# Optimization experiments

Measured on AMD Instinct MI355X. Metric: run time of the kernel, lower is better.

## Reference

```python
import jax, jax.numpy as jnp
import numpy as np

NUM_GRAPHS = 128
NUM_LAYERS = 3
D_IN = 64
D_H = 64
D_OUT = 10
N_NODES = 100000
N_EDGES = 1000000


def segment_softmax(scores, seg, num_segments):
    # numerically stable softmax over variable-size segments (per-destination-node)
    m = jax.ops.segment_max(scores, seg, num_segments=num_segments)
    ex = jnp.exp(scores - m[seg])
    s = jax.ops.segment_sum(ex, seg, num_segments=num_segments)
    return ex / (s[seg] + 1e-16)


def setup_inputs() -> dict:
    key = jax.random.key(0)
    ks = jax.random.split(key, 16)
    x = jax.random.normal(ks[0], (N_NODES, D_IN), dtype=jnp.float32)
    edge_index = jax.random.randint(ks[1], (2, N_EDGES), 0, N_NODES, dtype=jnp.int32)
    batch = jnp.sort(jax.random.randint(ks[2], (N_NODES,), 0, NUM_GRAPHS, dtype=jnp.int32))
    s = 0.05
    # stacked per-layer TransformerConv params (input_dim == hidden_dim so shapes align)
    Wq = jax.random.normal(ks[3], (NUM_LAYERS, D_H, D_H), dtype=jnp.float32) * s
    bq = jnp.zeros((NUM_LAYERS, D_H), dtype=jnp.float32)
    Wk = jax.random.normal(ks[4], (NUM_LAYERS, D_H, D_H), dtype=jnp.float32) * s
    bk = jnp.zeros((NUM_LAYERS, D_H), dtype=jnp.float32)
    Wv = jax.random.normal(ks[5], (NUM_LAYERS, D_H, D_H), dtype=jnp.float32) * s
    bv = jnp.zeros((NUM_LAYERS, D_H), dtype=jnp.float32)
    Ws = jax.random.normal(ks[6], (NUM_LAYERS, D_H, D_H), dtype=jnp.float32) * s  # root/skip lin
    bs = jnp.zeros((NUM_LAYERS, D_H), dtype=jnp.float32)
    W1 = jax.random.normal(ks[7], (D_H, D_H), dtype=jnp.float32) * s
    b1 = jnp.zeros((D_H,), dtype=jnp.float32)
    W2 = jax.random.normal(ks[8], (D_H, D_OUT), dtype=jnp.float32) * s
    b2 = jnp.zeros((D_OUT,), dtype=jnp.float32)
    return {"x": x, "edge_index": edge_index, "batch": batch,
            "Wq": Wq, "bq": bq, "Wk": Wk, "bk": bk, "Wv": Wv, "bv": bv,
            "Ws": Ws, "bs": bs, "W1": W1, "b1": b1, "W2": W2, "b2": b2}


def reference(x, edge_index, batch, Wq, bq, Wk, bk, Wv, bv, Ws, bs, W1, b1, W2, b2):
    n = x.shape[0]
    src, dst = edge_index[0], edge_index[1]  # PyG: edge_index[0]=source j, [1]=target i
    scale = 1.0 / jnp.sqrt(jnp.asarray(D_H, x.dtype))
    h = x
    pooled = []
    for l in range(NUM_LAYERS):
        q = h @ Wq[l] + bq[l]          # [N, d] query of target node
        k = h @ Wk[l] + bk[l]          # [N, d] key of source node
        v = h @ Wv[l] + bv[l]          # [N, d] value of source node
        scores = jnp.sum(q[dst] * k[src], axis=-1) * scale          # [E]
        alpha = segment_softmax(scores, dst, n)                     # softmax over in-edges
        agg = jax.ops.segment_sum(v[src] * alpha[:, None], dst, num_segments=n)  # [N, d]
        h = jax.nn.relu(agg + h @ Ws[l] + bs[l])                    # root_weight skip + relu
        pooled.append(jax.ops.segment_sum(h, batch, num_segments=NUM_GRAPHS))   # global_add_pool
    pooled_st = jnp.stack(pooled)                                   # [L, G, d]
    p = jax.nn.relu(pooled_st[-1] @ W1 + b1)                        # dropout p=0 / eval
    out = p @ W2 + b2                                               # [G, D_OUT]
    return out, pooled_st
```

## Files before the change

kernel.cpp:

```cpp
#include <hip/hip_runtime.h>
#include <hip/hip_bf16.h>
#include <math.h>

#define NN 100000
#define NE 1000000
#define DD 64
#define NG 128
#define NL 3

#define NBUK 196
#define EPB 2048
#define NBLK ((NE + EPB - 1) / EPB)
#define BCAP 6144
#define NDC 64

typedef unsigned short ushort_t;
typedef unsigned int u32;
typedef __attribute__((ext_vector_type(8))) short short8v;
typedef __attribute__((ext_vector_type(2))) float f32x2;
typedef __attribute__((ext_vector_type(4))) float f32x4;
typedef __attribute__((ext_vector_type(4))) unsigned int u32x4;

__device__ __forceinline__ ushort_t f2bf(float f) {
    __hip_bfloat16 h = __float2bfloat16(f);
    return *reinterpret_cast<ushort_t*>(&h);
}
__device__ __forceinline__ unsigned cvtpk(float lo, float hi) {
    unsigned r;
    asm("v_cvt_pk_bf16_f32 %0, %1, %2" : "=v"(r) : "v"(lo), "v"(hi));
    return r;
}
__device__ __forceinline__ f32x2 bfpair(u32 u) {
    f32x2 r;
    r.x = __builtin_bit_cast(float, u << 16);
    r.y = __builtin_bit_cast(float, u & 0xffff0000u);
    return r;
}
template <bool HI>
__device__ __forceinline__ f32x2 f8pair(u32 u) {
    return __builtin_amdgcn_cvt_pk_f32_fp8(u, HI);
}
__device__ __forceinline__ float sum8(float x) {
    int v = __builtin_bit_cast(int, x);
    x += __builtin_bit_cast(float, __builtin_amdgcn_update_dpp(0, v, 0xB1, 0xF, 0xF, true));
    v = __builtin_bit_cast(int, x);
    x += __builtin_bit_cast(float, __builtin_amdgcn_update_dpp(0, v, 0x4E, 0xF, 0xF, true));
    v = __builtin_bit_cast(int, x);
    x += __builtin_bit_cast(float, __builtin_amdgcn_update_dpp(0, v, 0x141, 0xF, 0xF, true));
    return x;
}


__global__ __launch_bounds__(256) void zero_k(float* __restrict__ out, int totOut,
                                              int* __restrict__ gcur, int* __restrict__ gdh) {
    int i = blockIdx.x * 256 + threadIdx.x;
    if (i < totOut) out[i] = 0.f;
    if (blockIdx.x == 0 && threadIdx.x < NBUK) gcur[threadIdx.x] = 0;
    if (blockIdx.x == 1 && threadIdx.x < NDC) gdh[threadIdx.x] = 0;
}


__global__ __launch_bounds__(256) void fused_k(const float* __restrict__ x, ushort_t* __restrict__ hbf,
                                               const float* __restrict__ Wq, const float* __restrict__ Wk,
                                               const float* __restrict__ Wv, const float* __restrict__ Ws_,
                                               ushort_t* __restrict__ wpack,
                                               const int* __restrict__ src, const int* __restrict__ dst,
                                               u32* __restrict__ binbuf, int* __restrict__ gcur,
                                               int cvtBlocks) {
    __shared__ int hist[NBUK];
    __shared__ int excl[NBUK];
    __shared__ int cur[NBUK];
    __shared__ int gbase[NBUK];
    __shared__ int tmp[256];
    __shared__ u32 pairs[EPB];
    __shared__ unsigned char bukid[EPB];

    int b = blockIdx.x, t = threadIdx.x;
    if (b < cvtBlocks) {
        int base = (b * 256 + t) * 4;
        float4 v = *(const float4*)&x[base];
        uint2 pk;
        pk.x = cvtpk(v.x, v.y);
        pk.y = cvtpk(v.z, v.w);
        *(uint2*)&hbf[base] = pk;
        return;
    }
    b -= cvtBlocks;
    if (b < NL * 4) {
        if (t < 64) {
            int mat = b & 3, layer = b >> 2;
            const float* W = ((mat == 0) ? Wq : (mat == 1) ? Wk : (mat == 2) ? Wv : Ws_) + layer * DD * DD;
#pragma unroll
            for (int ct = 0; ct < 4; ct++)
#pragma unroll
                for (int ks = 0; ks < 2; ks++)
#pragma unroll
                    for (int j = 0; j < 8; j++) {
                        float v = W[(ks * 32 + (t >> 4) * 8 + j) * DD + ct * 16 + (t & 15)];
                        wpack[((size_t)(b * 8 + ct * 2 + ks)) * 512 + t * 8 + j] = f2bf(v);
                    }
        }
        return;
    }
    b -= NL * 4;
    int e0 = b * EPB;
    int totvalid = NE - e0; if (totvalid > EPB) totvalid = EPB;

    for (int i = t; i < NBUK; i += 256) hist[i] = 0;
    __syncthreads();

    int mysrc[8], mydst[8];
#pragma unroll
    for (int i = 0; i < 8; i++) {
        int e = e0 + i * 256 + t;
        bool v = e < NE;
        mysrc[i] = v ? src[e] : -1;
        mydst[i] = v ? dst[e] : -1;
        if (v) atomicAdd(&hist[mydst[i] >> 9], 1);
    }
    __syncthreads();

    int v = (t < NBUK) ? hist[t] : 0;
    tmp[t] = v;
    __syncthreads();
#pragma unroll
    for (int off = 1; off < 256; off <<= 1) {
        int a = (t >= off) ? tmp[t - off] : 0;
        __syncthreads();
        tmp[t] += a;
        __syncthreads();
    }
    if (t < NBUK) { excl[t] = tmp[t] - v; cur[t] = tmp[t] - v; }
    __syncthreads();

#pragma unroll
    for (int i = 0; i < 8; i++) {
        if (mydst[i] >= 0) {
            int bb = mydst[i] >> 9;
            int p = atomicAdd(&cur[bb], 1);
            pairs[p] = ((u32)(mydst[i] & 511) << 17) | (u32)mysrc[i];
            bukid[p] = (unsigned char)bb;
        }
    }
    if (t < NBUK && v > 0) gbase[t] = atomicAdd(&gcur[t], v);
    __syncthreads();

    for (int i = t; i < totvalid; i += 256) {
        int bb = bukid[i];
        int idx = gbase[bb] + (i - excl[bb]);
        if (idx < BCAP) binbuf[(size_t)bb * BCAP + idx] = pairs[i];
    }
}


__global__ __launch_bounds__(256) void csr_k(const u32* __restrict__ binbuf,
                                             const int* __restrict__ gcur,
                                             int* __restrict__ rowstart,
                                             int* __restrict__ csr_src,
                                             int* __restrict__ gdh) {
    __shared__ u32 pairs[BCAP];
    __shared__ int csrb[BCAP];
    __shared__ int deg[512];
    __shared__ int excl[512];
    __shared__ int cur[512];
    __shared__ int tmp[512];
    __shared__ int bt[256];
    __shared__ int ch[NDC];
    int b = blockIdx.x;
    int t = threadIdx.x;

    int bv = 0;
    if (t < NBUK) { bv = gcur[t]; if (bv > BCAP) bv = BCAP; }
    bt[t] = bv;
    __syncthreads();
#pragma unroll
    for (int off = 1; off < 256; off <<= 1) {
        int a = (t >= off) ? bt[t - off] : 0;
        __syncthreads();
        bt[t] += a;
        __syncthreads();
    }
    int base = (b == 0) ? 0 : bt[b - 1];
    int T = bt[b] - base;
    if (b == 0 && t == 0) rowstart[NN] = bt[NBUK - 1];
    int nbase = b << 9;

    for (int i = t; i < 512; i += 256) deg[i] = 0;
    if (t < NDC) ch[t] = 0;
    for (int i = t; i < T; i += 256) pairs[i] = binbuf[(size_t)b * BCAP + i];
    __syncthreads();
    for (int i = t; i < T; i += 256) atomicAdd(&deg[pairs[i] >> 17], 1);
    __syncthreads();

    for (int i = t; i < 512; i += 256) {
        if (nbase + i < NN) {
            int d = deg[i]; if (d > NDC - 1) d = NDC - 1;
            atomicAdd(&ch[d], 1);
        }
    }

    int v0 = deg[t], v1 = deg[t + 256];
    tmp[t] = v0; tmp[t + 256] = v1;
    __syncthreads();
#pragma unroll
    for (int off = 1; off < 512; off <<= 1) {
        int a0 = (t >= off) ? tmp[t - off] : 0;
        int i1 = t + 256;
        int a1 = (i1 >= off) ? tmp[i1 - off] : 0;
        __syncthreads();
        tmp[t] += a0; tmp[i1] += a1;
        __syncthreads();
    }
    excl[t] = tmp[t] - v0; excl[t + 256] = tmp[t + 256] - v1;
    cur[t] = excl[t]; cur[t + 256] = excl[t + 256];
    if (t < NDC && ch[t]) atomicAdd(&gdh[t], ch[t]);
    __syncthreads();

    for (int i = t; i < 512; i += 256) {
        int n = nbase + i;
        if (n < NN) rowstart[n] = base + excl[i];
    }

    for (int i = t; i < T; i += 256) {
        u32 p = pairs[i];
        int pos = atomicAdd(&cur[p >> 17], 1);
        csrb[pos] = (int)(p & 0x1FFFFu);
    }
    __syncthreads();
    for (int i = t; i < T; i += 256) csr_src[base + i] = csrb[i];
}


__global__ __launch_bounds__(64) void dscan_k(const int* __restrict__ gdh,
                                              int* __restrict__ gdcur) {
    int t = threadIdx.x;
    int v = gdh[t];
    int inc = v;
#pragma unroll
    for (int off = 1; off < NDC; off <<= 1) {
        int u = __shfl_up(inc, off);
        if (t >= off) inc += u;
    }
    gdcur[t] = inc - v;
}

__global__ __launch_bounds__(256) void dperm_k(const int* __restrict__ rowstart,
                                               int* __restrict__ gdcur,
                                               int* __restrict__ perm) {
    __shared__ int h[NDC];
    __shared__ int cur[NDC];
    int t = threadIdx.x;
    if (t < NDC) h[t] = 0;
    __syncthreads();
    int n0 = blockIdx.x * 1024;
    int myd[4];
#pragma unroll
    for (int i = 0; i < 4; i++) {
        int n = n0 + i * 256 + t;
        myd[i] = -1;
        if (n < NN) {
            int d = rowstart[n + 1] - rowstart[n];
            if (d > NDC - 1) d = NDC - 1;
            myd[i] = d;
            atomicAdd(&h[d], 1);
        }
    }
    __syncthreads();
    if (t < NDC) cur[t] = h[t] ? atomicAdd(&gdcur[t], h[t]) : 0;
    __syncthreads();
#pragma unroll
    for (int i = 0; i < 4; i++) {
        if (myd[i] >= 0) {
            int pos = atomicAdd(&cur[myd[i]], 1);
            perm[pos] = n0 + i * 256 + t;
        }
    }
}


__global__ __launch_bounds__(256) void gemm4_k(const ushort_t* __restrict__ hbf,
                                               const ushort_t* __restrict__ wpl,
                                               const float* __restrict__ bq_, const float* __restrict__ bk_,
                                               const float* __restrict__ bv_, const float* __restrict__ bs_,
                                               ushort_t* __restrict__ qo, unsigned char* __restrict__ kv8,
                                               ushort_t* __restrict__ so) {
    int t = threadIdx.x;
    int lane = t & 63, wv = t >> 6;
    int ln = lane & 15, lq = lane >> 4;
    int rowbase = blockIdx.x * 64;

    const float* bsel = (wv == 0) ? bq_ : (wv == 1) ? bk_ : (wv == 2) ? bv_ : bs_;
    ushort_t* osel    = (wv == 0) ? qo : so;
    int kvoff = (wv == 1) ? 0 : 64;

    short8v wfrag[4][2];
#pragma unroll
    for (int ct = 0; ct < 4; ct++)
#pragma unroll
        for (int ks = 0; ks < 2; ks++)
            wfrag[ct][ks] = *(const short8v*)&wpl[((size_t)(wv * 8 + ct * 2 + ks)) * 512 + lane * 8];

    float4 bias[4];
#pragma unroll
    for (int ct = 0; ct < 4; ct++) bias[ct] = *(const float4*)&bsel[ct * 16 + lq * 4];

#pragma unroll
    for (int rt = 0; rt < 4; rt++) {
        int grow = rowbase + rt * 16 + ln;
        bool rv = grow < NN;
        int gr = rv ? grow : NN - 1;
        short8v h0 = *(const short8v*)&hbf[(size_t)gr * DD + lq * 8];
        short8v h1 = *(const short8v*)&hbf[(size_t)gr * DD + 32 + lq * 8];
#pragma unroll
        for (int ct = 0; ct < 4; ct++) {
            f32x4 acc;
            acc[0] = bias[ct].x; acc[1] = bias[ct].y; acc[2] = bias[ct].z; acc[3] = bias[ct].w;
            acc = __builtin_amdgcn_mfma_f32_16x16x32_bf16(wfrag[ct][0], h0, acc, 0, 0, 0);
            acc = __builtin_amdgcn_mfma_f32_16x16x32_bf16(wfrag[ct][1], h1, acc, 0, 0, 0);
            if (rv) {
                if (wv == 1 || wv == 2) {
                    int pk8 = __builtin_amdgcn_cvt_pk_fp8_f32(acc[0], acc[1], 0, false);
                    pk8 = __builtin_amdgcn_cvt_pk_fp8_f32(acc[2], acc[3], pk8, true);
                    *(u32*)&kv8[(size_t)grow * 128 + kvoff + ct * 16 + lq * 4] = (u32)pk8;
                } else {
                    uint2 pk;
                    pk.x = cvtpk(acc[0], acc[1]);
                    pk.y = cvtpk(acc[2], acc[3]);
                    *(uint2*)&osel[(size_t)grow * DD + ct * 16 + lq * 4] = pk;
                }
            }
        }
    }
}


#define SCLOG2E 0.18033688011112042f

__global__ __launch_bounds__(256) void agg_k(const ushort_t* __restrict__ qb,
                                             const unsigned char* __restrict__ kv8,
                                             const ushort_t* __restrict__ skb,
                                             const int* __restrict__ rowstart,
                                             const int* __restrict__ csr_src,
                                             const int* __restrict__ perm,
                                             ushort_t* __restrict__ hout) {
    int wv = threadIdx.x >> 6, lane = threadIdx.x & 63;
    int g = lane >> 3, j = lane & 7, sub = g & 1;
    int slot = blockIdx.x * 16 + wv * 4 + (g >> 1);
    if (slot >= NN) return;
    int nid = perm[(NN - 1) - slot];
    int r0 = rowstart[nid];
    int r1 = rowstart[nid + 1];

    u32x4 qa = *(const u32x4*)(qb + ((u32)nid << 6) + ((u32)j << 3));
    f32x2 q0 = bfpair(qa.x), q1 = bfpair(qa.y), q2 = bfpair(qa.z), q3 = bfpair(qa.w);

    float m = -1.0e38f, se = 0.f;
    f32x2 a0 = {0.f, 0.f}, a1 = {0.f, 0.f}, a2 = {0.f, 0.f}, a3 = {0.f, 0.f};

    int clampE = r1 - 1; if (clampE < 0) clampE = 0;
    int e0 = r0 + sub, e1 = e0 + 2;
    int s0 = csr_src[e0 < clampE ? e0 : clampE];
    int s1 = csr_src[e1 < clampE ? e1 : clampE];
    uint2 k0 = *(const uint2*)(kv8 + (size_t)s0 * 128 + 8 * j);
    uint2 v0 = *(const uint2*)(kv8 + (size_t)s0 * 128 + 64 + 8 * j);
    uint2 k1 = *(const uint2*)(kv8 + (size_t)s1 * 128 + 8 * j);
    uint2 v1 = *(const uint2*)(kv8 + (size_t)s1 * 128 + 64 + 8 * j);

    while (__ballot(e0 < r1)) {
        int e2 = e1 + 2;
        int s2 = csr_src[e2 < clampE ? e2 : clampE];
        uint2 k2 = *(const uint2*)(kv8 + (size_t)s2 * 128 + 8 * j);
        uint2 v2 = *(const uint2*)(kv8 + (size_t)s2 * 128 + 64 + 8 * j);

        f32x2 dp2 = q0 * f8pair<false>(k0.x);
        dp2 += q1 * f8pair<true >(k0.x);
        dp2 += q2 * f8pair<false>(k0.y);
        dp2 += q3 * f8pair<true >(k0.y);
        float dp = sum8(dp2.x + dp2.y);

        float w = 0.f;
        if (e0 < r1) {
            float sc = dp * SCLOG2E;
            if (sc <= m + 11.5f) { w = exp2f(sc - m); }
            else {
                float cc = exp2f(m - sc);
                se *= cc; a0 *= cc; a1 *= cc; a2 *= cc; a3 *= cc;
                m = sc; w = 1.f;
            }
        }
        se += w;
        a0 += f8pair<false>(v0.x) * w;
        a1 += f8pair<true >(v0.x) * w;
        a2 += f8pair<false>(v0.y) * w;
        a3 += f8pair<true >(v0.y) * w;

        e0 = e1; e1 = e2;
        k0 = k1; v0 = v1; k1 = k2; v1 = v2;
    }

    float M = fmaxf(m, __shfl_xor(m, 8));
    float cc = exp2f(m - M);
    se *= cc; a0 *= cc; a1 *= cc; a2 *= cc; a3 *= cc;
    se += __shfl_xor(se, 8);
    a0.x += __shfl_xor(a0.x, 8); a0.y += __shfl_xor(a0.y, 8);
    a1.x += __shfl_xor(a1.x, 8); a1.y += __shfl_xor(a1.y, 8);
    a2.x += __shfl_xor(a2.x, 8); a2.y += __shfl_xor(a2.y, 8);
    a3.x += __shfl_xor(a3.x, 8); a3.y += __shfl_xor(a3.y, 8);

    if (sub == 0) {
        float inv = 1.0f / (se + 1e-16f);
        u32x4 sk = *(const u32x4*)(skb + ((u32)nid << 6) + ((u32)j << 3));
        f32x2 o0 = a0 * inv + bfpair(sk.x);
        f32x2 o1 = a1 * inv + bfpair(sk.y);
        f32x2 o2 = a2 * inv + bfpair(sk.z);
        f32x2 o3 = a3 * inv + bfpair(sk.w);
        u32x4 pk;
        pk.x = cvtpk(fmaxf(o0.x, 0.f), fmaxf(o0.y, 0.f));
        pk.y = cvtpk(fmaxf(o1.x, 0.f), fmaxf(o1.y, 0.f));
        pk.z = cvtpk(fmaxf(o2.x, 0.f), fmaxf(o2.y, 0.f));
        pk.w = cvtpk(fmaxf(o3.x, 0.f), fmaxf(o3.y, 0.f));
        *(u32x4*)(hout + ((u32)nid << 6) + ((u32)j << 3)) = pk;
    }
}


#define POOL_ROWS 128

__global__ __launch_bounds__(256) void pool_k(const ushort_t* __restrict__ h,
                                              const int* __restrict__ batch,
                                              float* __restrict__ pooled) {
    int i0 = blockIdx.x * POOL_ROWS;
    int i1 = i0 + POOL_ROWS; if (i1 > NN) i1 = NN;
    int lane = threadIdx.x & 63;
    int wv = threadIdx.x >> 6;
    float acc = 0.f;
    int gcur = -1;
    for (int i = i0 + wv; i < i1; i += 4) {
        int gi = batch[i];
        if (gi != gcur) {
            if (gcur >= 0) atomicAdd(&pooled[gcur * DD + lane], acc);
            gcur = gi; acc = 0.f;
        }
        unsigned u = ((unsigned)h[(size_t)i * DD + lane]) << 16;
        acc += __builtin_bit_cast(float, u);
    }
    if (gcur >= 0) atomicAdd(&pooled[gcur * DD + lane], acc);
}


__global__ __launch_bounds__(64) void head_k(const float* __restrict__ pooled2,
                                             const float* __restrict__ W1,
                                             const float* __restrict__ b1,
                                             const float* __restrict__ W2,
                                             const float* __restrict__ b2,
                                             float* __restrict__ out) {
    int g = blockIdx.x;
    int c = threadIdx.x;
    __shared__ float pg[64], p[64];
    pg[c] = pooled2[g * DD + c];
    __syncthreads();
    float a = b1[c];
#pragma unroll 8
    for (int kk = 0; kk < 64; kk++) a += pg[kk] * W1[kk * DD + c];
    p[c] = fmaxf(a, 0.f);
    __syncthreads();
    if (c < 10) {
        float o = b2[c];
#pragma unroll 8
        for (int kk = 0; kk < 64; kk++) o += p[kk] * W2[kk * 10 + c];
        out[g * 10 + c] = o;
    }
}


extern "C" void kernel_launch(void* const* d_in, const int* in_sizes, int n_in,
                              void* d_out, int out_size, void* d_ws, size_t ws_size,
                              hipStream_t stream) {
    const float* x    = (const float*)d_in[0];
    const int*   ei   = (const int*)d_in[1];
    const int*   batch= (const int*)d_in[2];
    const float* Wq   = (const float*)d_in[3];
    const float* bq   = (const float*)d_in[4];
    const float* Wk   = (const float*)d_in[5];
    const float* bk   = (const float*)d_in[6];
    const float* Wv   = (const float*)d_in[7];
    const float* bv   = (const float*)d_in[8];
    const float* Wsp  = (const float*)d_in[9];
    const float* bsp  = (const float*)d_in[10];
    const float* W1   = (const float*)d_in[11];
    const float* b1   = (const float*)d_in[12];
    const float* W2   = (const float*)d_in[13];
    const float* b2   = (const float*)d_in[14];
    float* out = (float*)d_out;
    float* pooled = out + NG * 10;

    const int* srcv = ei;
    const int* dstv = ei + NE;

    const size_t NEL = (size_t)NN * DD;
    ushort_t* hbf = (ushort_t*)d_ws;
    ushort_t* qb  = hbf + NEL;
    ushort_t* skb = qb  + NEL;
    unsigned char* kv8 = (unsigned char*)(skb + NEL);
    u32* binbuf   = (u32*)(kv8 + (size_t)NN * 128);
    int* gcur     = (int*)(binbuf + (size_t)NBUK * BCAP);
    int* gdh      = gcur + NBUK;
    int* gdcur    = gdh + NDC;
    int* rowstart = gdcur + NDC;
    int* csr_src  = rowstart + (NN + 1);
    int* perm     = csr_src + NE;
    ushort_t* wpack = (ushort_t*)(perm + NN);

    int totOut = NG * 10 + NL * NG * DD;
    int cvtBlocks = (int)(NEL / 4 / 256);
    int zeroBlocks = (totOut + 255) / 256;

    zero_k<<<zeroBlocks, 256, 0, stream>>>(out, totOut, gcur, gdh);
    fused_k<<<cvtBlocks + NL * 4 + NBLK, 256, 0, stream>>>(
        x, hbf, Wq, Wk, Wv, Wsp, wpack, srcv, dstv, binbuf, gcur, cvtBlocks);
    csr_k<<<NBUK, 256, 0, stream>>>(binbuf, gcur, rowstart, csr_src, gdh);
    dscan_k<<<1, 64, 0, stream>>>(gdh, gdcur);
    dperm_k<<<(NN + 1023) / 1024, 256, 0, stream>>>(rowstart, gdcur, perm);

    int gtiles = (NN + 63) / 64;
    int poolblocks = (NN + POOL_ROWS - 1) / POOL_ROWS;
    for (int l = 0; l < NL; l++) {
        gemm4_k<<<gtiles, 256, 0, stream>>>(hbf, wpack + (size_t)l * 4 * 8 * 512,
                                            bq + l * DD, bk + l * DD, bv + l * DD, bsp + l * DD,
                                            qb, kv8, skb);
        agg_k<<<(NN + 15) / 16, 256, 0, stream>>>(qb, kv8, skb, rowstart, csr_src, perm, hbf);
        pool_k<<<poolblocks, 256, 0, stream>>>(hbf, batch, pooled + l * NG * DD);
    }
    head_k<<<NG, 64, 0, stream>>>(pooled + 2 * NG * DD, W1, b1, W2, b2, out);
}
```

Before: 253.0 us.

## Fuse pooling into next-layer GEMM launch and unroll edge aggregation by two

```diff
diff --git a/kernel.cpp b/kernel.cpp
--- a/kernel.cpp
+++ b/kernel.cpp
@@ -13,6 +13,7 @@
 #define NBLK ((NE + EPB - 1) / EPB)
 #define BCAP 6144
 #define NDC 64
+#define POOL_ROWS 128
 
 typedef unsigned short ushort_t;
 typedef unsigned int u32;
@@ -51,10 +52,7 @@
 }
 
 
-__global__ __launch_bounds__(256) void zero_k(float* __restrict__ out, int totOut,
-                                              int* __restrict__ gcur, int* __restrict__ gdh) {
-    int i = blockIdx.x * 256 + threadIdx.x;
-    if (i < totOut) out[i] = 0.f;
+__global__ __launch_bounds__(256) void zero_k(int* __restrict__ gcur, int* __restrict__ gdh) {
     if (blockIdx.x == 0 && threadIdx.x < NBUK) gcur[threadIdx.x] = 0;
     if (blockIdx.x == 1 && threadIdx.x < NDC) gdh[threadIdx.x] = 0;
 }
@@ -66,6 +64,7 @@
                                                ushort_t* __restrict__ wpack,
                                                const int* __restrict__ src, const int* __restrict__ dst,
                                                u32* __restrict__ binbuf, int* __restrict__ gcur,
+                                               float* __restrict__ out, int totOut,
                                                int cvtBlocks) {
     __shared__ int hist[NBUK];
     __shared__ int excl[NBUK];
@@ -103,6 +102,11 @@
         return;
     }
     b -= NL * 4;
+    if (b >= NBLK) {
+        int i = (b - NBLK) * 256 + t;
+        if (i < totOut) out[i] = 0.f;
+        return;
+    }
     int e0 = b * EPB;
     int totvalid = NE - e0; if (totvalid > EPB) totvalid = EPB;
 
@@ -278,16 +282,45 @@
 }
 
 
-__global__ __launch_bounds__(256) void gemm4_k(const ushort_t* __restrict__ hbf,
-                                               const ushort_t* __restrict__ wpl,
-                                               const float* __restrict__ bq_, const float* __restrict__ bk_,
-                                               const float* __restrict__ bv_, const float* __restrict__ bs_,
-                                               ushort_t* __restrict__ qo, unsigned char* __restrict__ kv8,
-                                               ushort_t* __restrict__ so) {
+__device__ __forceinline__ void pool_body(const ushort_t* __restrict__ h,
+                                          const int* __restrict__ batch,
+                                          float* __restrict__ pooled, int pb) {
+    int i0 = pb * POOL_ROWS;
+    int i1 = i0 + POOL_ROWS; if (i1 > NN) i1 = NN;
+    int lane = threadIdx.x & 63;
+    int wv = threadIdx.x >> 6;
+    float acc = 0.f;
+    int gc = -1;
+    for (int i = i0 + wv; i < i1; i += 4) {
+        int gi = batch[i];
+        if (gi != gc) {
+            if (gc >= 0) atomicAdd(&pooled[gc * DD + lane], acc);
+            gc = gi; acc = 0.f;
+        }
+        unsigned u = ((unsigned)h[(size_t)i * DD + lane]) << 16;
+        acc += __builtin_bit_cast(float, u);
+    }
+    if (gc >= 0) atomicAdd(&pooled[gc * DD + lane], acc);
+}
+
+
+__global__ __launch_bounds__(256) void gemm4pool_k(const ushort_t* __restrict__ hbf,
+                                                   const ushort_t* __restrict__ wpl,
+                                                   const float* __restrict__ bq_, const float* __restrict__ bk_,
+                                                   const float* __restrict__ bv_, const float* __restrict__ bs_,
+                                                   ushort_t* __restrict__ qo, unsigned char* __restrict__ kv8,
+                                                   ushort_t* __restrict__ so,
+                                                   const int* __restrict__ batch,
+                                                   float* __restrict__ pooledPrev, int gtiles) {
+    int blk = blockIdx.x;
+    if (blk >= gtiles) {
+        pool_body(hbf, batch, pooledPrev, blk - gtiles);
+        return;
+    }
     int t = threadIdx.x;
     int lane = t & 63, wv = t >> 6;
     int ln = lane & 15, lq = lane >> 4;
-    int rowbase = blockIdx.x * 64;
+    int rowbase = blk * 64;
 
     const float* bsel = (wv == 0) ? bq_ : (wv == 1) ? bk_ : (wv == 2) ? bv_ : bs_;
     ushort_t* osel    = (wv == 0) ? qo : so;
@@ -358,44 +391,72 @@
     f32x2 a0 = {0.f, 0.f}, a1 = {0.f, 0.f}, a2 = {0.f, 0.f}, a3 = {0.f, 0.f};
 
     int clampE = r1 - 1; if (clampE < 0) clampE = 0;
-    int e0 = r0 + sub, e1 = e0 + 2;
-    int s0 = csr_src[e0 < clampE ? e0 : clampE];
-    int s1 = csr_src[e1 < clampE ? e1 : clampE];
-    uint2 k0 = *(const uint2*)(kv8 + (size_t)s0 * 128 + 8 * j);
-    uint2 v0 = *(const uint2*)(kv8 + (size_t)s0 * 128 + 64 + 8 * j);
-    uint2 k1 = *(const uint2*)(kv8 + (size_t)s1 * 128 + 8 * j);
-    uint2 v1 = *(const uint2*)(kv8 + (size_t)s1 * 128 + 64 + 8 * j);
-
-    while (__ballot(e0 < r1)) {
-        int e2 = e1 + 2;
-        int s2 = csr_src[e2 < clampE ? e2 : clampE];
-        uint2 k2 = *(const uint2*)(kv8 + (size_t)s2 * 128 + 8 * j);
-        uint2 v2 = *(const uint2*)(kv8 + (size_t)s2 * 128 + 64 + 8 * j);
-
-        f32x2 dp2 = q0 * f8pair<false>(k0.x);
-        dp2 += q1 * f8pair<true >(k0.x);
-        dp2 += q2 * f8pair<false>(k0.y);
-        dp2 += q3 * f8pair<true >(k0.y);
-        float dp = sum8(dp2.x + dp2.y);
-
-        float w = 0.f;
-        if (e0 < r1) {
-            float sc = dp * SCLOG2E;
-            if (sc <= m + 11.5f) { w = exp2f(sc - m); }
-            else {
-                float cc = exp2f(m - sc);
+    int e = r0 + sub * 2;
+    int sA0 = csr_src[e     < clampE ? e     : clampE];
+    int sA1 = csr_src[e + 1 < clampE ? e + 1 : clampE];
+    int sB0 = csr_src[e + 4 < clampE ? e + 4 : clampE];
+    int sB1 = csr_src[e + 5 < clampE ? e + 5 : clampE];
+    int sC0 = csr_src[e + 8 < clampE ? e + 8 : clampE];
+    int sC1 = csr_src[e + 9 < clampE ? e + 9 : clampE];
+    int sD0 = csr_src[e + 12 < clampE ? e + 12 : clampE];
+    int sD1 = csr_src[e + 13 < clampE ? e + 13 : clampE];
+    uint2 kA0 = *(const uint2*)(kv8 + (size_t)sA0 * 128 + 8 * j);
+    uint2 vA0 = *(const uint2*)(kv8 + (size_t)sA0 * 128 + 64 + 8 * j);
+    uint2 kA1 = *(const uint2*)(kv8 + (size_t)sA1 * 128 + 8 * j);
+    uint2 vA1 = *(const uint2*)(kv8 + (size_t)sA1 * 128 + 64 + 8 * j);
+    uint2 kB0 = *(const uint2*)(kv8 + (size_t)sB0 * 128 + 8 * j);
+    uint2 vB0 = *(const uint2*)(kv8 + (size_t)sB0 * 128 + 64 + 8 * j);
+    uint2 kB1 = *(const uint2*)(kv8 + (size_t)sB1 * 128 + 8 * j);
+    uint2 vB1 = *(const uint2*)(kv8 + (size_t)sB1 * 128 + 64 + 8 * j);
+
+    while (__ballot(e < r1)) {
+        int e16 = e + 16;
+        int sE0 = csr_src[e16     < clampE ? e16     : clampE];
+        int sE1 = csr_src[e16 + 1 < clampE ? e16 + 1 : clampE];
+        uint2 kC0 = *(const uint2*)(kv8 + (size_t)sC0 * 128 + 8 * j);
+        uint2 vC0 = *(const uint2*)(kv8 + (size_t)sC0 * 128 + 64 + 8 * j);
+        uint2 kC1 = *(const uint2*)(kv8 + (size_t)sC1 * 128 + 8 * j);
+        uint2 vC1 = *(const uint2*)(kv8 + (size_t)sC1 * 128 + 64 + 8 * j);
+
+        f32x2 d0 = q0 * f8pair<false>(kA0.x);
+        d0 += q1 * f8pair<true >(kA0.x);
+        d0 += q2 * f8pair<false>(kA0.y);
+        d0 += q3 * f8pair<true >(kA0.y);
+        f32x2 d1 = q0 * f8pair<false>(kA1.x);
+        d1 += q1 * f8pair<true >(kA1.x);
+        d1 += q2 * f8pair<false>(kA1.y);
+        d1 += q3 * f8pair<true >(kA1.y);
+        float dp0 = sum8(d0.x + d0.y);
+        float dp1 = sum8(d1.x + d1.y);
+
+        bool act0 = e < r1, act1 = e + 1 < r1;
+        float sc0 = dp0 * SCLOG2E, sc1 = dp1 * SCLOG2E;
+        float s0a = act0 ? sc0 : -1.0e38f;
+        float s1a = act1 ? sc1 : -1.0e38f;
+        float pm = fmaxf(s0a, s1a);
+        float w0 = 0.f, w1 = 0.f;
+        if (pm > -1.0e37f) {
+            if (pm <= m + 11.5f) {
+                if (act0) w0 = exp2f(sc0 - m);
+                if (act1) w1 = exp2f(sc1 - m);
+            } else {
+                float cc = exp2f(m - pm);
                 se *= cc; a0 *= cc; a1 *= cc; a2 *= cc; a3 *= cc;
-                m = sc; w = 1.f;
+                m = pm;
+                if (act0) w0 = exp2f(sc0 - pm);
+                if (act1) w1 = exp2f(sc1 - pm);
             }
         }
-        se += w;
-        a0 += f8pair<false>(v0.x) * w;
-        a1 += f8pair<true >(v0.x) * w;
-        a2 += f8pair<false>(v0.y) * w;
-        a3 += f8pair<true >(v0.y) * w;
-
-        e0 = e1; e1 = e2;
-        k0 = k1; v0 = v1; k1 = k2; v1 = v2;
+        se += w0 + w1;
+        a0 += f8pair<false>(vA0.x) * w0 + f8pair<false>(vA1.x) * w1;
+        a1 += f8pair<true >(vA0.x) * w0 + f8pair<true >(vA1.x) * w1;
+        a2 += f8pair<false>(vA0.y) * w0 + f8pair<false>(vA1.y) * w1;
+        a3 += f8pair<true >(vA0.y) * w0 + f8pair<true >(vA1.y) * w1;
+
+        e += 4;
+        sC0 = sD0; sC1 = sD1; sD0 = sE0; sD1 = sE1;
+        kA0 = kB0; vA0 = vB0; kA1 = kB1; vA1 = vB1;
+        kB0 = kC0; vB0 = vC0; kB1 = kC1; vB1 = vC1;
     }
 
     float M = fmaxf(m, __shfl_xor(m, 8));
@@ -424,27 +485,10 @@
 }
 
 
-#define POOL_ROWS 128
-
 __global__ __launch_bounds__(256) void pool_k(const ushort_t* __restrict__ h,
                                               const int* __restrict__ batch,
                                               float* __restrict__ pooled) {
-    int i0 = blockIdx.x * POOL_ROWS;
-    int i1 = i0 + POOL_ROWS; if (i1 > NN) i1 = NN;
-    int lane = threadIdx.x & 63;
-    int wv = threadIdx.x >> 6;
-    float acc = 0.f;
-    int gcur = -1;
-    for (int i = i0 + wv; i < i1; i += 4) {
-        int gi = batch[i];
-        if (gi != gcur) {
-            if (gcur >= 0) atomicAdd(&pooled[gcur * DD + lane], acc);
-            gcur = gi; acc = 0.f;
-        }
-        unsigned u = ((unsigned)h[(size_t)i * DD + lane]) << 16;
-        acc += __builtin_bit_cast(float, u);
-    }
-    if (gcur >= 0) atomicAdd(&pooled[gcur * DD + lane], acc);
+    pool_body(h, batch, pooled, blockIdx.x);
 }
 
 
@@ -515,9 +559,9 @@
     int cvtBlocks = (int)(NEL / 4 / 256);
     int zeroBlocks = (totOut + 255) / 256;
 
-    zero_k<<<zeroBlocks, 256, 0, stream>>>(out, totOut, gcur, gdh);
-    fused_k<<<cvtBlocks + NL * 4 + NBLK, 256, 0, stream>>>(
-        x, hbf, Wq, Wk, Wv, Wsp, wpack, srcv, dstv, binbuf, gcur, cvtBlocks);
+    zero_k<<<2, 256, 0, stream>>>(gcur, gdh);
+    fused_k<<<cvtBlocks + NL * 4 + NBLK + zeroBlocks, 256, 0, stream>>>(
+        x, hbf, Wq, Wk, Wv, Wsp, wpack, srcv, dstv, binbuf, gcur, out, totOut, cvtBlocks);
     csr_k<<<NBUK, 256, 0, stream>>>(binbuf, gcur, rowstart, csr_src, gdh);
     dscan_k<<<1, 64, 0, stream>>>(gdh, gdcur);
     dperm_k<<<(NN + 1023) / 1024, 256, 0, stream>>>(rowstart, gdcur, perm);
@@ -525,11 +569,14 @@
     int gtiles = (NN + 63) / 64;
     int poolblocks = (NN + POOL_ROWS - 1) / POOL_ROWS;
     for (int l = 0; l < NL; l++) {
-        gemm4_k<<<gtiles, 256, 0, stream>>>(hbf, wpack + (size_t)l * 4 * 8 * 512,
-                                            bq + l * DD, bk + l * DD, bv + l * DD, bsp + l * DD,
-                                            qb, kv8, skb);
+        int extra = (l > 0) ? poolblocks : 0;
+        gemm4pool_k<<<gtiles + extra, 256, 0, stream>>>(
+            hbf, wpack + (size_t)l * 4 * 8 * 512,
+            bq + l * DD, bk + l * DD, bv + l * DD, bsp + l * DD,
+            qb, kv8, skb, batch,
+            (l > 0) ? (pooled + (l - 1) * NG * DD) : nullptr, gtiles);
         agg_k<<<(NN + 15) / 16, 256, 0, stream>>>(qb, kv8, skb, rowstart, csr_src, perm, hbf);
-        pool_k<<<poolblocks, 256, 0, stream>>>(hbf, batch, pooled + l * NG * DD);
-    }
+    }
+    pool_k<<<poolblocks, 256, 0, stream>>>(hbf, batch, pooled + 2 * NG * DD);
     head_k<<<NG, 64, 0, stream>>>(pooled + 2 * NG * DD, W1, b1, W2, b2, out);
 }
```

After: 236.3 us. -6.6%, faster.
